# Kernel tuning notes

Measured on AMD Instinct MI355X. Metric: run time of the kernel, lower is better.

Reference implementation:

```python
import jax, jax.numpy as jnp
import numpy as np

BN_EPS = 1e-5
NORM_EPS = 1e-12  # torch F.normalize eps


def setup_inputs() -> dict:
    key = jax.random.key(0)
    ks = jax.random.split(key, 7)
    B, N, D, K = 32, 4096, 512, 64
    init_sc = 1.0 / np.sqrt(D)
    x = jax.random.normal(ks[0], (B, N, D), dtype=jnp.float32)
    clusters = init_sc * jax.random.normal(ks[1], (D, K), dtype=jnp.float32)
    clusters2 = init_sc * jax.random.normal(ks[2], (1, D, K), dtype=jnp.float32)
    bn_weight = jax.random.uniform(ks[3], (K,), dtype=jnp.float32, minval=0.5, maxval=1.5)
    bn_bias = 0.1 * jax.random.normal(ks[4], (K,), dtype=jnp.float32)
    running_mean = 0.1 * jax.random.normal(ks[5], (K,), dtype=jnp.float32)
    running_var = jax.random.uniform(ks[6], (K,), dtype=jnp.float32, minval=0.5, maxval=1.5)
    return {"x": x, "clusters": clusters, "clusters2": clusters2,
            "bn_weight": bn_weight, "bn_bias": bn_bias,
            "running_mean": running_mean, "running_var": running_var}


def reference(x, clusters, clusters2, bn_weight, bn_bias, running_mean, running_var):
    B, N, D = x.shape
    K = clusters2.shape[2]
    x_flat = x.reshape(-1, D)                              # (B*N) x D
    logits = x_flat @ clusters                             # (B*N) x (K+G)
    # BatchNorm1d in eval mode: use running stats
    inv_std = jax.lax.rsqrt(running_var + BN_EPS)
    logits = (logits - running_mean) * inv_std * bn_weight + bn_bias
    assignment = jax.nn.softmax(logits, axis=1)[:, :K]     # drop ghost clusters
    assignment = assignment.reshape(B, N, K)
    a_sum = assignment.sum(axis=1, keepdims=True)
    a = a_sum * clusters2                                  # B x D x K
    vlad = jnp.einsum('bnk,bnd->bdk', assignment, x) - a   # B x D x K
    # intra-normalization over D (torch F.normalize dim=1)
    vlad = vlad / jnp.maximum(jnp.linalg.norm(vlad, axis=1, keepdims=True), NORM_EPS)
    vlad = vlad.reshape(B, D * K)
    vlad = vlad / jnp.maximum(jnp.linalg.norm(vlad, axis=1, keepdims=True), NORM_EPS)
    return vlad
```

## Files before the change

### kernel.cpp

```cpp
#include <hip/hip_runtime.h>
#include <stdint.h>

#define B_ 32
#define N_ 4096
#define D_ 512
#define K_ 64
#define M_ (B_ * N_)
#define NSPLIT 8

typedef float f32x4 __attribute__((ext_vector_type(4)));
typedef short bf16x8 __attribute__((ext_vector_type(8)));
typedef uint32_t u32;

union U8 { u32 u[4]; bf16x8 v; uint4 q4; };

__device__ __forceinline__ u32 pack_hi2(float a, float b) {
    return __builtin_amdgcn_perm(__float_as_uint(b), __float_as_uint(a), 0x07060302u);
}
__device__ __forceinline__ u32 lo16s(u32 p0, u32 p1) {
    return __builtin_amdgcn_perm(p1, p0, 0x05040100u);
}
__device__ __forceinline__ u32 hi16s(u32 p0, u32 p1) {
    return __builtin_amdgcn_perm(p1, p0, 0x07060302u);
}
__device__ __forceinline__ float trunc_hi(float f) {
    return __uint_as_float(__float_as_uint(f) & 0xffff0000u);
}

__global__ void k_prep(const float* __restrict__ clusters,
                       bf16x8* __restrict__ cfh, bf16x8* __restrict__ cfl)
{
    const int t = blockIdx.x;
    const int c = blockIdx.y;
    const int lane = threadIdx.x;
    const int q = lane >> 4, li = lane & 15;
    U8 h, l;
    #pragma unroll
    for (int j2 = 0; j2 < 4; ++j2) {
        float v0 = clusters[(t*32 + q*8 + 2*j2 + 0) * K_ + c*16 + li];
        float v1 = clusters[(t*32 + q*8 + 2*j2 + 1) * K_ + c*16 + li];
        float l0 = v0 - trunc_hi(v0), l1 = v1 - trunc_hi(v1);
        h.u[j2] = pack_hi2(v0, v1);
        l.u[j2] = pack_hi2(l0, l1);
    }
    cfh[(t*4 + c)*64 + lane] = h.v;
    cfl[(t*4 + c)*64 + lane] = l.v;
}

__global__ __launch_bounds__(256) void k_assign(
    const float* __restrict__ x,
    const bf16x8* __restrict__ cfh, const bf16x8* __restrict__ cfl,
    const float* __restrict__ bnw, const float* __restrict__ bnb,
    const float* __restrict__ rm, const float* __restrict__ rv,
    u32* __restrict__ asgT, float* __restrict__ a_sum)
{
    const int tid = threadIdx.x;
    const int w = tid >> 6, lane = tid & 63;
    const int q = lane >> 4, li = lane & 15;
    const int rbase = blockIdx.x * 128 + w * 32;

    __shared__ __align__(16) u32 asgT_lds[64][132];
    __shared__ float red[4][64];

    f32x4 acc[2][4];
    #pragma unroll
    for (int i = 0; i < 2; ++i)
        #pragma unroll
        for (int j = 0; j < 4; ++j) acc[i][j] = (f32x4){0.f, 0.f, 0.f, 0.f};

    for (int t = 0; t < 16; ++t) {
        bf16x8 bh[4], bl[4];
        #pragma unroll
        for (int c = 0; c < 4; ++c) {
            bh[c] = cfh[(t*4 + c)*64 + lane];
            bl[c] = cfl[(t*4 + c)*64 + lane];
        }
        #pragma unroll
        for (int mt = 0; mt < 2; ++mt) {
            const float* xp = x + (size_t)(rbase + mt*16 + li) * D_ + t*32 + q*8;
            float v[8];
            *(float4*)&v[0] = *(const float4*)xp;
            *(float4*)&v[4] = *(const float4*)(xp + 4);
            float lo[8];
            #pragma unroll
            for (int j = 0; j < 8; ++j) lo[j] = v[j] - trunc_hi(v[j]);
            U8 ah, al;
            #pragma unroll
            for (int j2 = 0; j2 < 4; ++j2) {
                ah.u[j2] = pack_hi2(v[2*j2], v[2*j2+1]);
                al.u[j2] = pack_hi2(lo[2*j2], lo[2*j2+1]);
            }
            #pragma unroll
            for (int c = 0; c < 4; ++c) {
                acc[mt][c] = __builtin_amdgcn_mfma_f32_16x16x32_bf16(ah.v, bh[c], acc[mt][c], 0, 0, 0);
                acc[mt][c] = __builtin_amdgcn_mfma_f32_16x16x32_bf16(ah.v, bl[c], acc[mt][c], 0, 0, 0);
                acc[mt][c] = __builtin_amdgcn_mfma_f32_16x16x32_bf16(al.v, bh[c], acc[mt][c], 0, 0, 0);
            }
        }
    }

    float alpha[4], beta[4];
    #pragma unroll
    for (int c = 0; c < 4; ++c) {
        const int col = c*16 + li;
        const float a = bnw[col] * rsqrtf(rv[col] + 1e-5f);
        alpha[c] = a;
        beta[c]  = bnb[col] - rm[col] * a;
    }

    float rs[4] = {0.f, 0.f, 0.f, 0.f};
    #pragma unroll
    for (int mt = 0; mt < 2; ++mt) {
        u32 pr[4][4];
        #pragma unroll
        for (int reg = 0; reg < 4; ++reg) {
            float lg[4];
            #pragma unroll
            for (int c = 0; c < 4; ++c) lg[c] = fmaf(acc[mt][c][reg], alpha[c], beta[c]);
            float mx = fmaxf(fmaxf(lg[0], lg[1]), fmaxf(lg[2], lg[3]));
            #pragma unroll
            for (int m = 1; m <= 8; m <<= 1) mx = fmaxf(mx, __shfl_xor(mx, m));
            float e[4], s = 0.f;
            #pragma unroll
            for (int c = 0; c < 4; ++c) { e[c] = __expf(lg[c] - mx); s += e[c]; }
            #pragma unroll
            for (int m = 1; m <= 8; m <<= 1) s += __shfl_xor(s, m);
            const float inv = 1.0f / s;
            #pragma unroll
            for (int c = 0; c < 4; ++c) {
                const float a = e[c] * inv;
                rs[c] += a;
                const float alo = a - trunc_hi(a);
                pr[reg][c] = pack_hi2(a, alo);
            }
        }
        #pragma unroll
        for (int c = 0; c < 4; ++c) {
            *(uint4*)&asgT_lds[c*16 + li][w*32 + mt*16 + q*4] =
                make_uint4(pr[0][c], pr[1][c], pr[2][c], pr[3][c]);
        }
    }

    #pragma unroll
    for (int c = 0; c < 4; ++c) {
        rs[c] += __shfl_xor(rs[c], 16);
        rs[c] += __shfl_xor(rs[c], 32);
    }
    if (q == 0) {
        #pragma unroll
        for (int c = 0; c < 4; ++c) red[w][c*16 + li] = rs[c];
    }
    __syncthreads();
    if (tid < 64) {
        const float s = red[0][tid] + red[1][tid] + red[2][tid] + red[3][tid];
        atomicAdd(&a_sum[(blockIdx.x >> 5) * K_ + tid], s);
    }

    const size_t ncol0 = (size_t)blockIdx.x * 128;
    #pragma unroll
    for (int l = 0; l < 8; ++l) {
        const int ii = tid + 256*l;
        const int k = ii >> 5, seg = ii & 31;
        const uint4 vv = *(const uint4*)&asgT_lds[k][seg*4];
        *(uint4*)&asgT[(size_t)k * M_ + ncol0 + seg*4] = vv;
    }
}

__global__ __launch_bounds__(256) void k_vlad(
    const float* __restrict__ x, const u32* __restrict__ asgT,
    float* __restrict__ part)
{
    const int tid = threadIdx.x;
    const int w = tid >> 6, lane = tid & 63;
    const int q = lane >> 4, li = lane & 15;
    const int s  = blockIdx.x;
    const int db = blockIdx.y;
    const int b  = blockIdx.z;
    const int d0 = db*256 + w*64;
    const int nbb = b * N_ + s * (N_ / NSPLIT);

    f32x4 acc[4][4];
    #pragma unroll
    for (int i = 0; i < 4; ++i)
        #pragma unroll
        for (int j = 0; j < 4; ++j) acc[i][j] = (f32x4){0.f, 0.f, 0.f, 0.f};

    for (int ch = 0; ch < (N_ / NSPLIT) / 32; ++ch) {
        const int nb = ch*32 + q*8;
        bf16x8 ah[4], al[4];
        #pragma unroll
        for (int mt = 0; mt < 4; ++mt) {
            const u32* ap = asgT + (size_t)(mt*16 + li) * M_ + nbb + nb;
            u32 p[8];
            *(uint4*)&p[0] = *(const uint4*)ap;
            *(uint4*)&p[4] = *(const uint4*)(ap + 4);
            U8 uh, ul;
            #pragma unroll
            for (int j2 = 0; j2 < 4; ++j2) {
                uh.u[j2] = lo16s(p[2*j2], p[2*j2+1]);
                ul.u[j2] = hi16s(p[2*j2], p[2*j2+1]);
            }
            ah[mt] = uh.v; al[mt] = ul.v;
        }
        #pragma unroll
        for (int nt = 0; nt < 4; ++nt) {
            const float* xp = x + (size_t)(nbb + nb) * D_ + d0 + nt*16 + li;
            float v[8];
            #pragma unroll
            for (int j = 0; j < 8; ++j) v[j] = xp[(size_t)j * D_];
            float lo[8];
            #pragma unroll
            for (int j = 0; j < 8; ++j) lo[j] = v[j] - trunc_hi(v[j]);
            U8 bh, bl;
            #pragma unroll
            for (int j2 = 0; j2 < 4; ++j2) {
                bh.u[j2] = pack_hi2(v[2*j2], v[2*j2+1]);
                bl.u[j2] = pack_hi2(lo[2*j2], lo[2*j2+1]);
            }
            #pragma unroll
            for (int mt = 0; mt < 4; ++mt) {
                acc[mt][nt] = __builtin_amdgcn_mfma_f32_16x16x32_bf16(ah[mt], bh.v, acc[mt][nt], 0, 0, 0);
                acc[mt][nt] = __builtin_amdgcn_mfma_f32_16x16x32_bf16(ah[mt], bl.v, acc[mt][nt], 0, 0, 0);
                acc[mt][nt] = __builtin_amdgcn_mfma_f32_16x16x32_bf16(al[mt], bh.v, acc[mt][nt], 0, 0, 0);
            }
        }
    }

    float* pp = part + ((size_t)s * B_ + b) * ((size_t)K_ * D_);
    #pragma unroll
    for (int mt = 0; mt < 4; ++mt)
        #pragma unroll
        for (int nt = 0; nt < 4; ++nt) {
            const int d = d0 + nt*16 + li;
            #pragma unroll
            for (int reg = 0; reg < 4; ++reg) {
                const int k = mt*16 + q*4 + reg;
                pp[(size_t)k * D_ + d] = acc[mt][nt][reg];
            }
        }
}

__global__ __launch_bounds__(256) void k_final1(
    const float* __restrict__ part_ro, const float* __restrict__ a_sum,
    const float* __restrict__ c2, float* __restrict__ part0,
    float* __restrict__ ssqk)
{
    const int b = blockIdx.x, dc = blockIdx.y;
    const int tid = threadIdx.x;
    const int k = tid >> 2, ds = tid & 3;
    const int d0 = dc*64 + ds*16;
    const float ak = a_sum[b*K_ + k];
    const size_t PS = (size_t)B_ * K_ * D_;
    const size_t base = ((size_t)b * K_ + k) * D_ + d0;
    float ssq = 0.f;
    #pragma unroll
    for (int i = 0; i < 4; ++i) {
        float4 v = *(const float4*)(part_ro + base + i*4);
        #pragma unroll
        for (int s = 1; s < NSPLIT; ++s) {
            const float4 p = *(const float4*)(part_ro + s*PS + base + i*4);
            v.x += p.x; v.y += p.y; v.z += p.z; v.w += p.w;
        }
        const int d = d0 + i*4;
        v.x = fmaf(-ak, c2[(d+0)*K_ + k], v.x);
        v.y = fmaf(-ak, c2[(d+1)*K_ + k], v.y);
        v.z = fmaf(-ak, c2[(d+2)*K_ + k], v.z);
        v.w = fmaf(-ak, c2[(d+3)*K_ + k], v.w);
        ssq = fmaf(v.x, v.x, fmaf(v.y, v.y, fmaf(v.z, v.z, fmaf(v.w, v.w, ssq))));
        *(float4*)(part0 + base + i*4) = v;
    }
    ssq += __shfl_xor(ssq, 1);
    ssq += __shfl_xor(ssq, 2);
    if (ds == 0) atomicAdd(&ssqk[b*K_ + k], ssq);
}

__global__ __launch_bounds__(256) void k_final2(
    const float* __restrict__ v0, const float* __restrict__ ssqk,
    float* __restrict__ out)
{
    const int b = blockIdx.x, dc = blockIdx.y;
    const int tid = threadIdx.x;
    __shared__ float T[64][65];
    __shared__ float invk[64];
    __shared__ float invg_s;

    if (tid < 64) {
        const float ss = ssqk[b*K_ + tid];
        const float inv = 1.0f / fmaxf(sqrtf(ss), 1e-12f);
        invk[tid] = inv;
        float gp = ss * inv * inv;
        #pragma unroll
        for (int m = 1; m < 64; m <<= 1) gp += __shfl_xor(gp, m);
        if (tid == 0) invg_s = 1.0f / fmaxf(sqrtf(gp), 1e-12f);
    }
    __syncthreads();

    const int k = tid >> 2, ds = tid & 3;
    const float sc = invk[k] * invg_s;
    const size_t base = ((size_t)b * K_ + k) * D_ + dc*64 + ds*16;
    #pragma unroll
    for (int i = 0; i < 4; ++i) {
        float4 v = *(const float4*)(v0 + base + i*4);
        const int dd = ds*16 + i*4;
        T[k][dd+0] = v.x * sc;
        T[k][dd+1] = v.y * sc;
        T[k][dd+2] = v.z * sc;
        T[k][dd+3] = v.w * sc;
    }
    __syncthreads();

    const int k2 = tid & 63, dl = tid >> 6;
    #pragma unroll
    for (int i = 0; i < 16; ++i) {
        const int dd = dl*16 + i;
        out[((size_t)b * D_ + dc*64 + dd) * K_ + k2] = T[k2][dd];
    }
}

extern "C" void kernel_launch(void* const* d_in, const int* in_sizes, int n_in,
                              void* d_out, int out_size, void* d_ws, size_t ws_size,
                              hipStream_t stream)
{
    const float* x    = (const float*)d_in[0];
    const float* clus = (const float*)d_in[1];
    const float* c2   = (const float*)d_in[2];
    const float* bnw  = (const float*)d_in[3];
    const float* bnb  = (const float*)d_in[4];
    const float* rm   = (const float*)d_in[5];
    const float* rv   = (const float*)d_in[6];
    float* out = (float*)d_out;

    u32*   asgT  = (u32*)d_ws;
    float* part  = (float*)(asgT + (size_t)K_ * M_);
    float* a_sum = part + (size_t)NSPLIT * B_ * K_ * D_;
    float* ssqk  = a_sum + B_ * K_;
    bf16x8* cfh  = (bf16x8*)(ssqk + B_ * K_);
    bf16x8* cfl  = cfh + 16*4*64;

    hipMemsetAsync(a_sum, 0, 2 * B_ * K_ * sizeof(float), stream);

    k_prep<<<dim3(16, 4), 64, 0, stream>>>(clus, cfh, cfl);
    k_assign<<<dim3(M_ / 128), 256, 0, stream>>>(x, cfh, cfl, bnw, bnb, rm, rv, asgT, a_sum);
    k_vlad<<<dim3(NSPLIT, 2, B_), 256, 0, stream>>>(x, asgT, part);
    k_final1<<<dim3(B_, 8), 256, 0, stream>>>(part, a_sum, c2, part, ssqk);
    k_final2<<<dim3(B_, 8), 256, 0, stream>>>(part, ssqk, out);
}
```

Measured before the change: 464.1 us.

## Fuse soft-assignment and VLAD aggregation into one LDS-staged kernel

The separate assignment and VLAD kernels are merged into one kernel. Each block stages 32-token tiles of x in swizzled LDS using global_load_lds, computes the softmax assignments, and immediately accumulates the assignment-by-x product from the same tile. This removes the second full read of x and the round-trip of the transposed assignment buffer through global memory. The softmax now skips max subtraction, which risks overflow for large logits. The N split doubles to 16, and the finalize kernels are retiled for more blocks, at the cost of more partial-sum traffic. Tile loads are synchronous and not double-buffered, so load latency is exposed between chunks.

```diff
diff --git a/kernel.cpp b/kernel.cpp
--- a/kernel.cpp
+++ b/kernel.cpp
@@ -6,7 +6,8 @@
 #define D_ 512
 #define K_ 64
 #define M_ (B_ * N_)
-#define NSPLIT 8
+#define NS 16
+#define CPB 8
 
 typedef float f32x4 __attribute__((ext_vector_type(4)));
 typedef short bf16x8 __attribute__((ext_vector_type(8)));
@@ -25,6 +26,16 @@
 }
 __device__ __forceinline__ float trunc_hi(float f) {
     return __uint_as_float(__float_as_uint(f) & 0xffff0000u);
+}
+
+__device__ __forceinline__ void gload16(const void* g, void* l) {
+    __builtin_amdgcn_global_load_lds(
+        (const __attribute__((address_space(1))) u32*)g,
+        (__attribute__((address_space(3))) u32*)l, 16, 0, 0);
+}
+
+__device__ __forceinline__ int xswb(int tok) {
+    return ((tok & 7) ^ (tok >> 3)) << 4;
 }
 
 __global__ void k_prep(const float* __restrict__ clusters,
@@ -47,197 +58,193 @@
     cfl[(t*4 + c)*64 + lane] = l.v;
 }
 
-__global__ __launch_bounds__(256) void k_assign(
+__global__ __launch_bounds__(256, 2) void k_fused(
     const float* __restrict__ x,
     const bf16x8* __restrict__ cfh, const bf16x8* __restrict__ cfl,
     const float* __restrict__ bnw, const float* __restrict__ bnb,
     const float* __restrict__ rm, const float* __restrict__ rv,
-    u32* __restrict__ asgT, float* __restrict__ a_sum)
-{
-    const int tid = threadIdx.x;
-    const int w = tid >> 6, lane = tid & 63;
-    const int q = lane >> 4, li = lane & 15;
-    const int rbase = blockIdx.x * 128 + w * 32;
-
-    __shared__ __align__(16) u32 asgT_lds[64][132];
-    __shared__ float red[4][64];
-
-    f32x4 acc[2][4];
-    #pragma unroll
-    for (int i = 0; i < 2; ++i)
-        #pragma unroll
-        for (int j = 0; j < 4; ++j) acc[i][j] = (f32x4){0.f, 0.f, 0.f, 0.f};
-
-    for (int t = 0; t < 16; ++t) {
-        bf16x8 bh[4], bl[4];
-        #pragma unroll
-        for (int c = 0; c < 4; ++c) {
-            bh[c] = cfh[(t*4 + c)*64 + lane];
-            bl[c] = cfl[(t*4 + c)*64 + lane];
-        }
-        #pragma unroll
-        for (int mt = 0; mt < 2; ++mt) {
-            const float* xp = x + (size_t)(rbase + mt*16 + li) * D_ + t*32 + q*8;
-            float v[8];
-            *(float4*)&v[0] = *(const float4*)xp;
-            *(float4*)&v[4] = *(const float4*)(xp + 4);
-            float lo[8];
-            #pragma unroll
-            for (int j = 0; j < 8; ++j) lo[j] = v[j] - trunc_hi(v[j]);
-            U8 ah, al;
-            #pragma unroll
-            for (int j2 = 0; j2 < 4; ++j2) {
-                ah.u[j2] = pack_hi2(v[2*j2], v[2*j2+1]);
-                al.u[j2] = pack_hi2(lo[2*j2], lo[2*j2+1]);
-            }
-            #pragma unroll
-            for (int c = 0; c < 4; ++c) {
-                acc[mt][c] = __builtin_amdgcn_mfma_f32_16x16x32_bf16(ah.v, bh[c], acc[mt][c], 0, 0, 0);
-                acc[mt][c] = __builtin_amdgcn_mfma_f32_16x16x32_bf16(ah.v, bl[c], acc[mt][c], 0, 0, 0);
-                acc[mt][c] = __builtin_amdgcn_mfma_f32_16x16x32_bf16(al.v, bh[c], acc[mt][c], 0, 0, 0);
-            }
-        }
-    }
-
-    float alpha[4], beta[4];
-    #pragma unroll
-    for (int c = 0; c < 4; ++c) {
-        const int col = c*16 + li;
+    float* __restrict__ part, float* __restrict__ a_sum)
+{
+    const int tid  = threadIdx.x;
+    const int w    = tid >> 6, lane = tid & 63;
+    const int q    = lane >> 4, li = lane & 15;
+    const int mt   = w >> 1, chp = w & 1;
+    const int s    = blockIdx.x, b = blockIdx.y;
+    const size_t n0 = (size_t)b * N_ + (size_t)s * (N_ / NS);
+
+    __shared__ __align__(16) float xt[32 * 512];
+    __shared__ __align__(16) u32  at[64 * 32];
+    __shared__ float red[32][2];
+
+    float alpha[2], beta[2];
+    #pragma unroll
+    for (int c = 0; c < 2; ++c) {
+        const int col = chp*32 + c*16 + li;
         const float a = bnw[col] * rsqrtf(rv[col] + 1e-5f);
         alpha[c] = a;
         beta[c]  = bnb[col] - rm[col] * a;
     }
 
-    float rs[4] = {0.f, 0.f, 0.f, 0.f};
-    #pragma unroll
-    for (int mt = 0; mt < 2; ++mt) {
-        u32 pr[4][4];
+    f32x4 acc[4][8];
+    #pragma unroll
+    for (int i = 0; i < 4; ++i)
+        #pragma unroll
+        for (int j = 0; j < 8; ++j) acc[i][j] = (f32x4){0.f, 0.f, 0.f, 0.f};
+    float rs[2] = {0.f, 0.f};
+
+    #pragma unroll
+    for (int i = 0; i < 16; ++i) {
+        const int offu   = (w << 14) + (i << 10);
+        const int tok    = offu >> 11;
+        const int within = (offu & 2047) + (lane << 4);
+        gload16((const char*)(x + (n0 + tok) * D_) + (within ^ xswb(tok)),
+                (char*)xt + offu);
+    }
+    __syncthreads();
+
+    for (int ch = 0; ch < CPB; ++ch) {
+        f32x4 lacc[2];
+        lacc[0] = (f32x4){0.f,0.f,0.f,0.f};
+        lacc[1] = (f32x4){0.f,0.f,0.f,0.f};
+        const int  tokA = mt*16 + li;
+        const char* xrow = (const char*)xt + tokA * 2048;
+        const int  swbA = xswb(tokA);
+        #pragma unroll
+        for (int t = 0; t < 16; ++t) {
+            const int lin = t*128 + q*32;
+            const uint4 r0 = *(const uint4*)(xrow + ( lin       ^ swbA));
+            const uint4 r1 = *(const uint4*)(xrow + ((lin + 16) ^ swbA));
+            float v[8];
+            v[0]=__uint_as_float(r0.x); v[1]=__uint_as_float(r0.y);
+            v[2]=__uint_as_float(r0.z); v[3]=__uint_as_float(r0.w);
+            v[4]=__uint_as_float(r1.x); v[5]=__uint_as_float(r1.y);
+            v[6]=__uint_as_float(r1.z); v[7]=__uint_as_float(r1.w);
+            float lo[8];
+            #pragma unroll
+            for (int j = 0; j < 8; ++j) lo[j] = v[j] - trunc_hi(v[j]);
+            U8 ah, al;
+            #pragma unroll
+            for (int j2 = 0; j2 < 4; ++j2) {
+                ah.u[j2] = pack_hi2(v[2*j2],  v[2*j2+1]);
+                al.u[j2] = pack_hi2(lo[2*j2], lo[2*j2+1]);
+            }
+            #pragma unroll
+            for (int c = 0; c < 2; ++c) {
+                const int idx = (t*4 + chp*2 + c)*64 + lane;
+                const bf16x8 bh = cfh[idx], bl = cfl[idx];
+                lacc[c] = __builtin_amdgcn_mfma_f32_16x16x32_bf16(ah.v, bh, lacc[c], 0, 0, 0);
+                lacc[c] = __builtin_amdgcn_mfma_f32_16x16x32_bf16(ah.v, bl, lacc[c], 0, 0, 0);
+                lacc[c] = __builtin_amdgcn_mfma_f32_16x16x32_bf16(al.v, bh, lacc[c], 0, 0, 0);
+            }
+        }
+        float e[2][4];
         #pragma unroll
         for (int reg = 0; reg < 4; ++reg) {
-            float lg[4];
-            #pragma unroll
-            for (int c = 0; c < 4; ++c) lg[c] = fmaf(acc[mt][c][reg], alpha[c], beta[c]);
-            float mx = fmaxf(fmaxf(lg[0], lg[1]), fmaxf(lg[2], lg[3]));
-            #pragma unroll
-            for (int m = 1; m <= 8; m <<= 1) mx = fmaxf(mx, __shfl_xor(mx, m));
-            float e[4], s = 0.f;
-            #pragma unroll
-            for (int c = 0; c < 4; ++c) { e[c] = __expf(lg[c] - mx); s += e[c]; }
-            #pragma unroll
-            for (int m = 1; m <= 8; m <<= 1) s += __shfl_xor(s, m);
-            const float inv = 1.0f / s;
-            #pragma unroll
-            for (int c = 0; c < 4; ++c) {
-                const float a = e[c] * inv;
+            float s0 = 0.f;
+            #pragma unroll
+            for (int c = 0; c < 2; ++c) {
+                const float lg = fmaf(lacc[c][reg], alpha[c], beta[c]);
+                e[c][reg] = __expf(lg);
+                s0 += e[c][reg];
+            }
+            #pragma unroll
+            for (int m = 1; m <= 8; m <<= 1) s0 += __shfl_xor(s0, m);
+            if (li == 0) red[mt*16 + q*4 + reg][chp] = s0;
+        }
+        __syncthreads();
+        #pragma unroll
+        for (int reg = 0; reg < 4; ++reg) {
+            const int tok = mt*16 + q*4 + reg;
+            const float inv = 1.0f / (red[tok][0] + red[tok][1]);
+            #pragma unroll
+            for (int c = 0; c < 2; ++c) {
+                const float a = e[c][reg] * inv;
                 rs[c] += a;
-                const float alo = a - trunc_hi(a);
-                pr[reg][c] = pack_hi2(a, alo);
-            }
-        }
-        #pragma unroll
-        for (int c = 0; c < 4; ++c) {
-            *(uint4*)&asgT_lds[c*16 + li][w*32 + mt*16 + q*4] =
-                make_uint4(pr[0][c], pr[1][c], pr[2][c], pr[3][c]);
-        }
-    }
-
-    #pragma unroll
-    for (int c = 0; c < 4; ++c) {
+                const int k = chp*32 + c*16 + li;
+                *(u32*)((char*)at + k*128 + ((tok*4) ^ ((k & 7) << 4))) =
+                    pack_hi2(a, a - trunc_hi(a));
+            }
+        }
+        __syncthreads();
+        bf16x8 ah2[4], al2[4];
+        #pragma unroll
+        for (int mtv = 0; mtv < 4; ++mtv) {
+            const int k = mtv*16 + li;
+            const char* arow = (const char*)at + k*128;
+            const int swb = (k & 7) << 4;
+            const uint4 p0 = *(const uint4*)(arow + ((q*32)      ^ swb));
+            const uint4 p1 = *(const uint4*)(arow + ((q*32 + 16) ^ swb));
+            U8 uh, ul;
+            uh.u[0] = lo16s(p0.x, p0.y); uh.u[1] = lo16s(p0.z, p0.w);
+            uh.u[2] = lo16s(p1.x, p1.y); uh.u[3] = lo16s(p1.z, p1.w);
+            ul.u[0] = hi16s(p0.x, p0.y); ul.u[1] = hi16s(p0.z, p0.w);
+            ul.u[2] = hi16s(p1.x, p1.y); ul.u[3] = hi16s(p1.z, p1.w);
+            ah2[mtv] = uh.v; al2[mtv] = ul.v;
+        }
+        const int d0 = w * 128;
+        #pragma unroll
+        for (int nt = 0; nt < 8; ++nt) {
+            const int dcol = d0 + nt*16 + li;
+            float v[8];
+            #pragma unroll
+            for (int j = 0; j < 8; ++j) {
+                const int tok = q*8 + j;
+                v[j] = *(const float*)((const char*)xt + tok*2048 +
+                        ((dcol*4) ^ xswb(tok)));
+            }
+            float lo[8];
+            #pragma unroll
+            for (int j = 0; j < 8; ++j) lo[j] = v[j] - trunc_hi(v[j]);
+            U8 bh, bl;
+            #pragma unroll
+            for (int j2 = 0; j2 < 4; ++j2) {
+                bh.u[j2] = pack_hi2(v[2*j2],  v[2*j2+1]);
+                bl.u[j2] = pack_hi2(lo[2*j2], lo[2*j2+1]);
+            }
+            #pragma unroll
+            for (int mtv = 0; mtv < 4; ++mtv) {
+                acc[mtv][nt] = __builtin_amdgcn_mfma_f32_16x16x32_bf16(ah2[mtv], bh.v, acc[mtv][nt], 0, 0, 0);
+                acc[mtv][nt] = __builtin_amdgcn_mfma_f32_16x16x32_bf16(ah2[mtv], bl.v, acc[mtv][nt], 0, 0, 0);
+                acc[mtv][nt] = __builtin_amdgcn_mfma_f32_16x16x32_bf16(al2[mtv], bh.v, acc[mtv][nt], 0, 0, 0);
+            }
+        }
+        __syncthreads();
+        if (ch + 1 < CPB) {
+            const size_t nbase = n0 + (size_t)(ch + 1) * 32;
+            #pragma unroll
+            for (int i = 0; i < 16; ++i) {
+                const int offu   = (w << 14) + (i << 10);
+                const int tok    = offu >> 11;
+                const int within = (offu & 2047) + (lane << 4);
+                gload16((const char*)(x + (nbase + tok) * D_) + (within ^ xswb(tok)),
+                        (char*)xt + offu);
+            }
+        }
+        __syncthreads();
+    }
+
+    float* pp = part + ((size_t)s * B_ + b) * ((size_t)K_ * D_);
+    #pragma unroll
+    for (int mtv = 0; mtv < 4; ++mtv)
+        #pragma unroll
+        for (int nt = 0; nt < 8; ++nt) {
+            const int dcol = w*128 + nt*16 + li;
+            #pragma unroll
+            for (int reg = 0; reg < 4; ++reg) {
+                const int k = mtv*16 + q*4 + reg;
+                pp[(size_t)k * D_ + dcol] = acc[mtv][nt][reg];
+            }
+        }
+    #pragma unroll
+    for (int c = 0; c < 2; ++c) {
         rs[c] += __shfl_xor(rs[c], 16);
         rs[c] += __shfl_xor(rs[c], 32);
     }
     if (q == 0) {
         #pragma unroll
-        for (int c = 0; c < 4; ++c) red[w][c*16 + li] = rs[c];
-    }
-    __syncthreads();
-    if (tid < 64) {
-        const float s = red[0][tid] + red[1][tid] + red[2][tid] + red[3][tid];
-        atomicAdd(&a_sum[(blockIdx.x >> 5) * K_ + tid], s);
-    }
-
-    const size_t ncol0 = (size_t)blockIdx.x * 128;
-    #pragma unroll
-    for (int l = 0; l < 8; ++l) {
-        const int ii = tid + 256*l;
-        const int k = ii >> 5, seg = ii & 31;
-        const uint4 vv = *(const uint4*)&asgT_lds[k][seg*4];
-        *(uint4*)&asgT[(size_t)k * M_ + ncol0 + seg*4] = vv;
-    }
-}
-
-__global__ __launch_bounds__(256) void k_vlad(
-    const float* __restrict__ x, const u32* __restrict__ asgT,
-    float* __restrict__ part)
-{
-    const int tid = threadIdx.x;
-    const int w = tid >> 6, lane = tid & 63;
-    const int q = lane >> 4, li = lane & 15;
-    const int s  = blockIdx.x;
-    const int db = blockIdx.y;
-    const int b  = blockIdx.z;
-    const int d0 = db*256 + w*64;
-    const int nbb = b * N_ + s * (N_ / NSPLIT);
-
-    f32x4 acc[4][4];
-    #pragma unroll
-    for (int i = 0; i < 4; ++i)
-        #pragma unroll
-        for (int j = 0; j < 4; ++j) acc[i][j] = (f32x4){0.f, 0.f, 0.f, 0.f};
-
-    for (int ch = 0; ch < (N_ / NSPLIT) / 32; ++ch) {
-        const int nb = ch*32 + q*8;
-        bf16x8 ah[4], al[4];
-        #pragma unroll
-        for (int mt = 0; mt < 4; ++mt) {
-            const u32* ap = asgT + (size_t)(mt*16 + li) * M_ + nbb + nb;
-            u32 p[8];
-            *(uint4*)&p[0] = *(const uint4*)ap;
-            *(uint4*)&p[4] = *(const uint4*)(ap + 4);
-            U8 uh, ul;
-            #pragma unroll
-            for (int j2 = 0; j2 < 4; ++j2) {
-                uh.u[j2] = lo16s(p[2*j2], p[2*j2+1]);
-                ul.u[j2] = hi16s(p[2*j2], p[2*j2+1]);
-            }
-            ah[mt] = uh.v; al[mt] = ul.v;
-        }
-        #pragma unroll
-        for (int nt = 0; nt < 4; ++nt) {
-            const float* xp = x + (size_t)(nbb + nb) * D_ + d0 + nt*16 + li;
-            float v[8];
-            #pragma unroll
-            for (int j = 0; j < 8; ++j) v[j] = xp[(size_t)j * D_];
-            float lo[8];
-            #pragma unroll
-            for (int j = 0; j < 8; ++j) lo[j] = v[j] - trunc_hi(v[j]);
-            U8 bh, bl;
-            #pragma unroll
-            for (int j2 = 0; j2 < 4; ++j2) {
-                bh.u[j2] = pack_hi2(v[2*j2], v[2*j2+1]);
-                bl.u[j2] = pack_hi2(lo[2*j2], lo[2*j2+1]);
-            }
-            #pragma unroll
-            for (int mt = 0; mt < 4; ++mt) {
-                acc[mt][nt] = __builtin_amdgcn_mfma_f32_16x16x32_bf16(ah[mt], bh.v, acc[mt][nt], 0, 0, 0);
-                acc[mt][nt] = __builtin_amdgcn_mfma_f32_16x16x32_bf16(ah[mt], bl.v, acc[mt][nt], 0, 0, 0);
-                acc[mt][nt] = __builtin_amdgcn_mfma_f32_16x16x32_bf16(al[mt], bh.v, acc[mt][nt], 0, 0, 0);
-            }
-        }
-    }
-
-    float* pp = part + ((size_t)s * B_ + b) * ((size_t)K_ * D_);
-    #pragma unroll
-    for (int mt = 0; mt < 4; ++mt)
-        #pragma unroll
-        for (int nt = 0; nt < 4; ++nt) {
-            const int d = d0 + nt*16 + li;
-            #pragma unroll
-            for (int reg = 0; reg < 4; ++reg) {
-                const int k = mt*16 + q*4 + reg;
-                pp[(size_t)k * D_ + d] = acc[mt][nt][reg];
-            }
-        }
+        for (int c = 0; c < 2; ++c)
+            atomicAdd(&a_sum[b*K_ + chp*32 + c*16 + li], rs[c]);
+    }
 }
 
 __global__ __launch_bounds__(256) void k_final1(
@@ -248,27 +255,22 @@
     const int b = blockIdx.x, dc = blockIdx.y;
     const int tid = threadIdx.x;
     const int k = tid >> 2, ds = tid & 3;
-    const int d0 = dc*64 + ds*16;
+    const int d = dc*16 + ds*4;
     const float ak = a_sum[b*K_ + k];
     const size_t PS = (size_t)B_ * K_ * D_;
-    const size_t base = ((size_t)b * K_ + k) * D_ + d0;
-    float ssq = 0.f;
-    #pragma unroll
-    for (int i = 0; i < 4; ++i) {
-        float4 v = *(const float4*)(part_ro + base + i*4);
-        #pragma unroll
-        for (int s = 1; s < NSPLIT; ++s) {
-            const float4 p = *(const float4*)(part_ro + s*PS + base + i*4);
-            v.x += p.x; v.y += p.y; v.z += p.z; v.w += p.w;
-        }
-        const int d = d0 + i*4;
-        v.x = fmaf(-ak, c2[(d+0)*K_ + k], v.x);
-        v.y = fmaf(-ak, c2[(d+1)*K_ + k], v.y);
-        v.z = fmaf(-ak, c2[(d+2)*K_ + k], v.z);
-        v.w = fmaf(-ak, c2[(d+3)*K_ + k], v.w);
-        ssq = fmaf(v.x, v.x, fmaf(v.y, v.y, fmaf(v.z, v.z, fmaf(v.w, v.w, ssq))));
-        *(float4*)(part0 + base + i*4) = v;
-    }
+    const size_t base = ((size_t)b * K_ + k) * D_ + d;
+    float4 v = *(const float4*)(part_ro + base);
+    #pragma unroll
+    for (int ss = 1; ss < NS; ++ss) {
+        const float4 p = *(const float4*)(part_ro + (size_t)ss*PS + base);
+        v.x += p.x; v.y += p.y; v.z += p.z; v.w += p.w;
+    }
+    v.x = fmaf(-ak, c2[(d+0)*K_ + k], v.x);
+    v.y = fmaf(-ak, c2[(d+1)*K_ + k], v.y);
+    v.z = fmaf(-ak, c2[(d+2)*K_ + k], v.z);
+    v.w = fmaf(-ak, c2[(d+3)*K_ + k], v.w);
+    float ssq = fmaf(v.x, v.x, fmaf(v.y, v.y, fmaf(v.z, v.z, v.w * v.w)));
+    *(float4*)(part0 + base) = v;
     ssq += __shfl_xor(ssq, 1);
     ssq += __shfl_xor(ssq, 2);
     if (ds == 0) atomicAdd(&ssqk[b*K_ + k], ssq);
@@ -280,7 +282,7 @@
 {
     const int b = blockIdx.x, dc = blockIdx.y;
     const int tid = threadIdx.x;
-    __shared__ float T[64][65];
+    __shared__ float T[64][33];
     __shared__ float invk[64];
     __shared__ float invg_s;
 
@@ -297,11 +299,11 @@
 
     const int k = tid >> 2, ds = tid & 3;
     const float sc = invk[k] * invg_s;
-    const size_t base = ((size_t)b * K_ + k) * D_ + dc*64 + ds*16;
-    #pragma unroll
-    for (int i = 0; i < 4; ++i) {
+    const size_t base = ((size_t)b * K_ + k) * D_ + dc*32 + ds*8;
+    #pragma unroll
+    for (int i = 0; i < 2; ++i) {
         float4 v = *(const float4*)(v0 + base + i*4);
-        const int dd = ds*16 + i*4;
+        const int dd = ds*8 + i*4;
         T[k][dd+0] = v.x * sc;
         T[k][dd+1] = v.y * sc;
         T[k][dd+2] = v.z * sc;
@@ -311,9 +313,9 @@
 
     const int k2 = tid & 63, dl = tid >> 6;
     #pragma unroll
-    for (int i = 0; i < 16; ++i) {
-        const int dd = dl*16 + i;
-        out[((size_t)b * D_ + dc*64 + dd) * K_ + k2] = T[k2][dd];
+    for (int i = 0; i < 8; ++i) {
+        const int dd = dl*8 + i;
+        out[((size_t)b * D_ + dc*32 + dd) * K_ + k2] = T[k2][dd];
     }
 }
 
@@ -330,9 +332,8 @@
     const float* rv   = (const float*)d_in[6];
     float* out = (float*)d_out;
 
-    u32*   asgT  = (u32*)d_ws;
-    float* part  = (float*)(asgT + (size_t)K_ * M_);
-    float* a_sum = part + (size_t)NSPLIT * B_ * K_ * D_;
+    float* part  = (float*)d_ws;
+    float* a_sum = part + (size_t)NS * B_ * K_ * D_;
     float* ssqk  = a_sum + B_ * K_;
     bf16x8* cfh  = (bf16x8*)(ssqk + B_ * K_);
     bf16x8* cfl  = cfh + 16*4*64;
@@ -340,8 +341,7 @@
     hipMemsetAsync(a_sum, 0, 2 * B_ * K_ * sizeof(float), stream);
 
     k_prep<<<dim3(16, 4), 64, 0, stream>>>(clus, cfh, cfl);
-    k_assign<<<dim3(M_ / 128), 256, 0, stream>>>(x, cfh, cfl, bnw, bnb, rm, rv, asgT, a_sum);
-    k_vlad<<<dim3(NSPLIT, 2, B_), 256, 0, stream>>>(x, asgT, part);
-    k_final1<<<dim3(B_, 8), 256, 0, stream>>>(part, a_sum, c2, part, ssqk);
-    k_final2<<<dim3(B_, 8), 256, 0, stream>>>(part, ssqk, out);
-}
+    k_fused<<<dim3(NS, B_), 256, 0, stream>>>(x, cfh, cfl, bnw, bnb, rm, rv, part, a_sum);
+    k_final1<<<dim3(B_, 32), 256, 0, stream>>>(part, a_sum, c2, part, ssqk);
+    k_final2<<<dim3(B_, 16), 256, 0, stream>>>(part, ssqk, out);
+}
```

Measured after the change: 791.8 us. +70.6%, slower.
